# Kernel tuning notes

Measured on AMD Instinct MI355X. Metric: run time of the kernel, lower is better.

## Reference

```python
import jax, jax.numpy as jnp
import numpy as np

B, L, E, H = 2048, 64, 128, 128  # batch, sourceL(=seq_len), lstm input dim (embedding_dim+2), hidden_dim
STEPS = (L - 1) * 2              # decode loop length from Decoder.forward
C_TANH = 10.0                    # tanh_exploration (pointer uses use_tanh=True)
NEG = -1e9                       # stand-in for -inf mask fill (grad-safe)


def setup_inputs() -> dict:
    key = jax.random.key(0)
    ks = jax.random.split(key, 20)
    s = 1.0 / np.sqrt(H)
    u = lambda k, shp: jax.random.uniform(k, shp, minval=-s, maxval=s, dtype=jnp.float32)
    return {
        'decoder_input': jax.random.normal(ks[0], (B, E), dtype=jnp.float32),
        'embedded_inputs': jax.random.normal(ks[1], (L, B, E), dtype=jnp.float32),
        'context': jax.random.normal(ks[2], (L, B, H), dtype=jnp.float32),
        'h0': jax.random.normal(ks[3], (B, H), dtype=jnp.float32),
        'c0': jax.random.normal(ks[4], (B, H), dtype=jnp.float32),
        # nn.LSTM(E, H) single-step cell params (PyTorch gate order i,f,g,o)
        'W_ih': u(ks[5], (4 * H, E)), 'W_hh': u(ks[6], (4 * H, H)),
        'b_ih': u(ks[7], (4 * H,)), 'b_hh': u(ks[8], (4 * H,)),
        # glimpse Attention (use_tanh=False): Linear(dim,dim), Conv1d(dim,dim,1), v
        'g_Wq': u(ks[9], (H, H)), 'g_bq': u(ks[10], (H,)),
        'g_Wref': u(ks[11], (H, H)), 'g_bref': u(ks[12], (H,)),
        'g_v': u(ks[13], (H,)),
        # pointer Attention (use_tanh=True, C=10)
        'p_Wq': u(ks[14], (H, H)), 'p_bq': u(ks[15], (H,)),
        'p_Wref': u(ks[16], (H, H)), 'p_bref': u(ks[17], (H,)),
        'p_v': u(ks[18], (H,)),
    }


def reference(decoder_input, embedded_inputs, context, h0, c0,
              W_ih, W_hh, b_ih, b_hh,
              g_Wq, g_bq, g_Wref, g_bref, g_v,
              p_Wq, p_bq, p_Wref, p_bref, p_v):
    # ref.permute(1,2,0): [sourceL,B,H] -> [B,H,L]; conv1d(dim,dim,1) == per-position linear.
    refT = jnp.transpose(context, (1, 2, 0))                                  # [B,H,L]
    e_g = jnp.einsum('oh,bhl->bol', g_Wref, refT) + g_bref[None, :, None]     # glimpse projected ref
    e_p = jnp.einsum('oh,bhl->bol', p_Wref, refT) + p_bref[None, :, None]     # pointer projected ref
    barange = jnp.arange(B)

    def step(carry, _):
        h, c, mask, idxs, x = carry
        # LSTM cell step (PyTorch i,f,g,o gate order)
        gates = x @ W_ih.T + h @ W_hh.T + (b_ih + b_hh)                       # [B,4H]
        i_, f_, g_, o_ = jnp.split(gates, 4, axis=1)
        c_new = jax.nn.sigmoid(f_) * c + jax.nn.sigmoid(i_) * jnp.tanh(g_)
        h_new = jax.nn.sigmoid(o_) * jnp.tanh(c_new)
        # apply_mask_to_logits: mark prev idxs, unmask depot (col 0) for non-depot prev
        mask = mask.at[barange, idxs].set(True)
        mask = mask.at[:, 0].set(jnp.where(idxs != 0, False, mask[:, 0]))
        # glimpse: additive attention, masked softmax, bmm with projected ref e
        qg = h_new @ g_Wq.T + g_bq                                            # [B,H]
        ug = jnp.einsum('h,bhl->bl', g_v, jnp.tanh(qg[:, :, None] + e_g))     # [B,L]
        ug = jnp.where(mask, NEG, ug)
        g_l = jnp.einsum('bhl,bl->bh', e_g, jax.nn.softmax(ug, axis=1))       # glimpse vector
        # pointer: additive attention with C*tanh, masked softmax
        qp = g_l @ p_Wq.T + p_bq
        up = jnp.einsum('h,bhl->bl', p_v, jnp.tanh(qp[:, :, None] + e_p))
        up = C_TANH * jnp.tanh(up)
        up = jnp.where(mask, NEG, up)
        probs = jax.nn.softmax(up, axis=1)                                    # [B,L]
        # selection (deterministic argmax stand-in for multinomial) + next decoder input
        new_idxs = jnp.argmax(probs, axis=1)
        x_new = embedded_inputs[new_idxs, barange, :]                         # [B,E]
        return (h_new, c_new, mask, new_idxs, x_new), probs

    mask0 = jnp.zeros((B, L), dtype=bool)
    idxs0 = jnp.zeros((B,), dtype=jnp.int32)
    _, probs_seq = jax.lax.scan(step, (h0, c0, mask0, idxs0, decoder_input), None, length=STEPS)
    prob0 = jnp.zeros((B, L), dtype=probs_seq.dtype).at[:, 0].set(1.0)        # initial depot one-hot
    return jnp.concatenate([prob0[None], probs_seq], axis=0)                  # [STEPS+1,B,L]
```

## Files before the change

kernel.cpp:

```cpp
#include <hip/hip_runtime.h>


#define B_ 2048
#define L_ 64
#define H_ 128
#define STEPS_ 126
#define NEGV -1000000000.0f

__device__ __forceinline__ float fast_rcp(float x) { return __builtin_amdgcn_rcpf(x); }
__device__ __forceinline__ float sigm(float x) { return 1.0f / (1.0f + __expf(-x)); }
__device__ __forceinline__ float dot4(float4 a, float4 b) {
  return a.x * b.x + a.y * b.y + a.z * b.z + a.w * b.w;
}

__global__ __launch_bounds__(256) void xw_gemm(const float* __restrict__ A,
                                               const float* __restrict__ W,
                                               const float* __restrict__ b1,
                                               const float* __restrict__ b2,
                                               float* __restrict__ C) {
  __shared__ float As[64][36];
  __shared__ float Ws[64][36];
  const int t = threadIdx.x;
  const int tx = t & 15, ty = t >> 4;
  const long row0 = (long)blockIdx.x * 64;
  const int col0 = blockIdx.y * 64;
  float acc[4][4] = {};
  for (int k0 = 0; k0 < 128; k0 += 32) {
#pragma unroll
    for (int i = 0; i < 2; ++i) {
      int f4 = t * 2 + i;
      int r = f4 >> 3, c = (f4 & 7) * 4;
      *(float4*)&As[r][c] = *(const float4*)&A[(row0 + r) * 128 + k0 + c];
      *(float4*)&Ws[r][c] = *(const float4*)&W[(long)(col0 + r) * 128 + k0 + c];
    }
    __syncthreads();
#pragma unroll
    for (int kk = 0; kk < 32; kk += 4) {
      float4 a[4], w[4];
#pragma unroll
      for (int i = 0; i < 4; ++i) a[i] = *(float4*)&As[ty * 4 + i][kk];
#pragma unroll
      for (int j = 0; j < 4; ++j) w[j] = *(float4*)&Ws[tx * 4 + j][kk];
#pragma unroll
      for (int i = 0; i < 4; ++i)
#pragma unroll
        for (int j = 0; j < 4; ++j)
          acc[i][j] += dot4(a[i], w[j]);
    }
    __syncthreads();
  }
#pragma unroll
  for (int i = 0; i < 4; ++i) {
    long r = row0 + ty * 4 + i;
#pragma unroll
    for (int j = 0; j < 4; ++j) {
      int cc = col0 + tx * 4 + j;
      C[r * 512 + cc] = acc[i][j] + b1[cc] + b2[cc];
    }
  }
}

__global__ __launch_bounds__(512, 1) void ptrnet_main(
    const float* __restrict__ dec, const float* __restrict__ emb,
    const float* __restrict__ ctx, const float* __restrict__ h0,
    const float* __restrict__ c0, const float* __restrict__ W_ih,
    const float* __restrict__ W_hh, const float* __restrict__ b_ih,
    const float* __restrict__ b_hh, const float* __restrict__ gWq,
    const float* __restrict__ gbq, const float* __restrict__ gWref,
    const float* __restrict__ gbref, const float* __restrict__ gv,
    const float* __restrict__ pWq, const float* __restrict__ pbq,
    const float* __restrict__ pWref, const float* __restrict__ pbref,
    const float* __restrict__ pv, const float* __restrict__ XW,
    const float* __restrict__ XW0, float* __restrict__ out, int use_precomp) {
  const int b = blockIdx.x;
  const int t = threadIdx.x;
  const int l = t & 63;
  const int hb = t >> 6;

  __shared__ float tegS[128][64];
  __shared__ float tepS[128][64];
  __shared__ float egT[64][128];
  __shared__ __align__(16) float hS[128];
  __shared__ float cS[128];
  __shared__ __align__(16) float glS[128];
  __shared__ __align__(16) float xS[128];
  __shared__ float gatesS[512];
  __shared__ __align__(16) float aG[128];
  __shared__ __align__(16) float gvaG[128];
  __shared__ __align__(16) float aP[128];
  __shared__ __align__(16) float pvaP[128];
  __shared__ __align__(16) float gvS[128];
  __shared__ __align__(16) float pvS[128];
  __shared__ float gbqS[128], pbqS[128];
  __shared__ float bS[512];
  __shared__ float wS[64];
  __shared__ float part[8][64];
  __shared__ float red4[4][128];
  __shared__ int maskS[64];
  __shared__ int curS;

  if (t < 128) {
    hS[t] = h0[(long)b * 128 + t];
    cS[t] = c0[(long)b * 128 + t];
    gvS[t] = gv[t];
    pvS[t] = pv[t];
    gbqS[t] = gbq[t];
    pbqS[t] = pbq[t];
  }
  bS[t] = b_ih[t] + b_hh[t];
  if (t < 64) {
    maskS[t] = 0;
    out[(long)b * 64 + t] = (t == 0) ? 1.0f : 0.0f;
  }
  if (t == 0) curS = 0;

  {
    const float4* crow4 = (const float4*)(ctx + ((long)l * B_ + b) * 128);
    for (int k = 0; k < 16; ++k) {
      int h = hb * 16 + k;
      float eg = gbref[h], ep = pbref[h];
      const float4* wg4 = (const float4*)(gWref + (long)h * 128);
      const float4* wp4 = (const float4*)(pWref + (long)h * 128);
#pragma unroll
      for (int c = 0; c < 32; ++c) {
        float4 cv = crow4[c];
        eg += dot4(cv, wg4[c]);
        ep += dot4(cv, wp4[c]);
      }
      egT[l][h] = eg;
      tegS[h][l] = tanhf(eg);
      tepS[h][l] = tanhf(ep);
    }
  }

  float4 whh[32];
  const float4* Whh4 = (const float4*)W_hh;
#pragma unroll
  for (int c = 0; c < 32; ++c) whh[c] = Whh4[(long)t * 32 + c];
  float4 qw[16];
  {
    const float4* Q4 = (t < 256) ? (const float4*)gWq : (const float4*)pWq;
    int j = (t & 255) >> 1, half = t & 1;
#pragma unroll
    for (int c = 0; c < 16; ++c) qw[c] = Q4[(long)j * 32 + half * 16 + c];
  }
  __syncthreads();

  const float4* hS4 = (const float4*)hS;
  const float4* glS4 = (const float4*)glS;
  const float4* xS4 = (const float4*)xS;
  float4* xS4w = (float4*)xS;

  for (int step = 0; step < STEPS_; ++step) {
    const int cur = curS;
    if (t == 0) {
      maskS[cur] = 1;
      if (cur != 0) maskS[0] = 0;
    }

    if (!use_precomp) {
      if (t < 32)
        xS4w[t] = (step == 0) ? ((const float4*)(dec + (long)b * 128))[t]
                              : ((const float4*)(emb + ((long)cur * B_ + b) * 128))[t];
      __syncthreads();
    }

    float xv;
    if (use_precomp) {
      const float* xw = (step == 0) ? (XW0 + (long)b * 512)
                                    : (XW + ((long)cur * B_ + b) * 512);
      xv = xw[t];
    } else {
      xv = bS[t];
      const float4* wih4 = (const float4*)(W_ih + (long)t * 128);
#pragma unroll
      for (int c = 0; c < 32; ++c) xv += dot4(wih4[c], xS4[c]);
    }
    {
      float acc = 0.f;
#pragma unroll
      for (int c = 0; c < 32; ++c) acc += dot4(whh[c], hS4[c]);
      gatesS[t] = acc + xv;
    }
    __syncthreads();

    if (t < 128) {
      float gi = gatesS[t], gf = gatesS[t + 128];
      float gg = gatesS[t + 256], go = gatesS[t + 384];
      float cn = sigm(gf) * cS[t] + sigm(gi) * tanhf(gg);
      cS[t] = cn;
      hS[t] = sigm(go) * tanhf(cn);
    }
    __syncthreads();

    if (t < 256) {
      int j = t >> 1, half = t & 1;
      float p = 0.f;
#pragma unroll
      for (int c = 0; c < 16; ++c) p += dot4(qw[c], hS4[half * 16 + c]);
      p += __shfl_xor(p, 1);
      if (half == 0) {
        float a = tanhf(p + gbqS[j]);
        aG[j] = a;
        gvaG[j] = gvS[j] * a;
      }
    }
    __syncthreads();

    {
      const float4* a4 = (const float4*)aG;
      const float4* g4 = (const float4*)gvS;
      const float4* ga4 = (const float4*)gvaG;
      float4 av[4], gv4[4], gav[4];
#pragma unroll
      for (int i = 0; i < 4; ++i) {
        av[i] = a4[hb * 4 + i];
        gv4[i] = g4[hb * 4 + i];
        gav[i] = ga4[hb * 4 + i];
      }
      const float* af = (const float*)av;
      const float* gf = (const float*)gv4;
      const float* gaf = (const float*)gav;
      float sum = 0.f;
#pragma unroll
      for (int k = 0; k < 16; ++k) {
        float te = tegS[hb * 16 + k][l];
        float den = fmaf(af[k], te, 1.0f);
        float n2 = fmaf(gf[k], te, gaf[k]);
        sum = fmaf(n2, fast_rcp(den), sum);
      }
      part[hb][l] = sum;
    }
    __syncthreads();

    if (t < 64) {
      float u = part[0][l] + part[1][l] + part[2][l] + part[3][l] +
                part[4][l] + part[5][l] + part[6][l] + part[7][l];
      if (maskS[l]) u = NEGV;
      float m = u;
#pragma unroll
      for (int d = 32; d; d >>= 1) m = fmaxf(m, __shfl_xor(m, d));
      float e = __expf(u - m);
      float s = e;
#pragma unroll
      for (int d = 32; d; d >>= 1) s += __shfl_xor(s, d);
      wS[l] = e / s;
    }
    __syncthreads();

    {
      int h = t & 127, lh = t >> 7;
      float sum = 0.f;
#pragma unroll
      for (int q = 0; q < 16; ++q) {
        int l2 = lh * 16 + q;
        sum = fmaf(egT[l2][h], wS[l2], sum);
      }
      red4[lh][h] = sum;
    }
    __syncthreads();
    if (t < 128) glS[t] = red4[0][t] + red4[1][t] + red4[2][t] + red4[3][t];
    __syncthreads();

    if (t >= 256) {
      int j = (t - 256) >> 1, half = t & 1;
      float p = 0.f;
#pragma unroll
      for (int c = 0; c < 16; ++c) p += dot4(qw[c], glS4[half * 16 + c]);
      p += __shfl_xor(p, 1);
      if (half == 0) {
        float a = tanhf(p + pbqS[j]);
        aP[j] = a;
        pvaP[j] = pvS[j] * a;
      }
    }
    __syncthreads();

    {
      const float4* a4 = (const float4*)aP;
      const float4* p4 = (const float4*)pvS;
      const float4* pa4 = (const float4*)pvaP;
      float4 av[4], pv4[4], pav[4];
#pragma unroll
      for (int i = 0; i < 4; ++i) {
        av[i] = a4[hb * 4 + i];
        pv4[i] = p4[hb * 4 + i];
        pav[i] = pa4[hb * 4 + i];
      }
      const float* af = (const float*)av;
      const float* pf = (const float*)pv4;
      const float* paf = (const float*)pav;
      float sum = 0.f;
#pragma unroll
      for (int k = 0; k < 16; ++k) {
        float te = tepS[hb * 16 + k][l];
        float den = fmaf(af[k], te, 1.0f);
        float n2 = fmaf(pf[k], te, paf[k]);
        sum = fmaf(n2, fast_rcp(den), sum);
      }
      part[hb][l] = sum;
    }
    __syncthreads();

    if (t < 64) {
      float u = part[0][l] + part[1][l] + part[2][l] + part[3][l] +
                part[4][l] + part[5][l] + part[6][l] + part[7][l];
      u = 10.0f * tanhf(u);
      if (maskS[l]) u = NEGV;
      float m = u;
#pragma unroll
      for (int d = 32; d; d >>= 1) m = fmaxf(m, __shfl_xor(m, d));
      float e = __expf(u - m);
      float s = e;
#pragma unroll
      for (int d = 32; d; d >>= 1) s += __shfl_xor(s, d);
      float p = e / s;
      out[((long)(step + 1) * B_ + b) * 64 + l] = p;
      float bv = p;
      int bi = l;
#pragma unroll
      for (int d = 32; d; d >>= 1) {
        float ov = __shfl_xor(bv, d);
        int oi = __shfl_xor(bi, d);
        if (ov > bv || (ov == bv && oi < bi)) { bv = ov; bi = oi; }
      }
      if (t == 0) curS = bi;
    }
    __syncthreads();
  }
}

extern "C" void kernel_launch(void* const* d_in, const int* in_sizes, int n_in,
                              void* d_out, int out_size, void* d_ws, size_t ws_size,
                              hipStream_t stream) {
  const float* dec = (const float*)d_in[0];
  const float* emb = (const float*)d_in[1];
  const float* ctx = (const float*)d_in[2];
  const float* h0 = (const float*)d_in[3];
  const float* c0 = (const float*)d_in[4];
  const float* Wih = (const float*)d_in[5];
  const float* Whh = (const float*)d_in[6];
  const float* bih = (const float*)d_in[7];
  const float* bhh = (const float*)d_in[8];
  const float* gWq = (const float*)d_in[9];
  const float* gbq = (const float*)d_in[10];
  const float* gWref = (const float*)d_in[11];
  const float* gbref = (const float*)d_in[12];
  const float* gv = (const float*)d_in[13];
  const float* pWq = (const float*)d_in[14];
  const float* pbq = (const float*)d_in[15];
  const float* pWref = (const float*)d_in[16];
  const float* pbref = (const float*)d_in[17];
  const float* pv = (const float*)d_in[18];
  float* out = (float*)d_out;

  const size_t xw_elems = (size_t)L_ * B_ * 512;
  const size_t need = (xw_elems + (size_t)B_ * 512) * sizeof(float);
  const int use_precomp = (ws_size >= need) ? 1 : 0;
  float* XW = (float*)d_ws;
  float* XW0 = XW + xw_elems;

  if (use_precomp) {
    dim3 g1((L_ * B_) / 64, 512 / 64);
    xw_gemm<<<g1, 256, 0, stream>>>(emb, Wih, bih, bhh, XW);
    dim3 g2(B_ / 64, 512 / 64);
    xw_gemm<<<g2, 256, 0, stream>>>(dec, Wih, bih, bhh, XW0);
  }
  ptrnet_main<<<dim3(B_), dim3(512), 0, stream>>>(
      dec, emb, ctx, h0, c0, Wih, Whh, bih, bhh, gWq, gbq, gWref, gbref, gv,
      pWq, pbq, pWref, pbref, pv, XW, XW0, out, use_precomp);
}
```

Baseline: 15.18 ms.

## Double block size to 1024 threads and split per-step dot products across more lanes

Each batch block now runs 1024 threads instead of 512. The LSTM gate products, query projections, attention sums and glimpse reduction are split over twice as many threads, with extra shuffles and shared-memory partial reductions. This cuts per-thread register arrays (whh from 32 to 16 float4) and should shorten the serial critical path of each decode step. The egT row is also padded to 129 to avoid bank conflicts. The cost is more threads per block, which limits concurrent blocks per CU, plus more reduction overhead at each synchronised step.

```diff
diff --git a/kernel.cpp b/kernel.cpp
--- a/kernel.cpp
+++ b/kernel.cpp
@@ -60,7 +60,7 @@
   }
 }
 
-__global__ __launch_bounds__(512, 1) void ptrnet_main(
+__global__ __launch_bounds__(1024) void ptrnet_main(
     const float* __restrict__ dec, const float* __restrict__ emb,
     const float* __restrict__ ctx, const float* __restrict__ h0,
     const float* __restrict__ c0, const float* __restrict__ W_ih,
@@ -74,12 +74,12 @@
     const float* __restrict__ XW0, float* __restrict__ out, int use_precomp) {
   const int b = blockIdx.x;
   const int t = threadIdx.x;
-  const int l = t & 63;
-  const int hb = t >> 6;
+  const int lane = t & 63;
+  const int wid = t >> 6;
 
   __shared__ float tegS[128][64];
   __shared__ float tepS[128][64];
-  __shared__ float egT[64][128];
+  __shared__ float egT[64][129];
   __shared__ __align__(16) float hS[128];
   __shared__ float cS[128];
   __shared__ __align__(16) float glS[128];
@@ -93,9 +93,9 @@
   __shared__ __align__(16) float pvS[128];
   __shared__ float gbqS[128], pbqS[128];
   __shared__ float bS[512];
-  __shared__ float wS[64];
-  __shared__ float part[8][64];
-  __shared__ float red4[4][128];
+  __shared__ __align__(16) float wS[64];
+  __shared__ float part2[16][64];
+  __shared__ float red8[8][128];
   __shared__ int maskS[64];
   __shared__ int curS;
 
@@ -107,7 +107,7 @@
     gbqS[t] = gbq[t];
     pbqS[t] = pbq[t];
   }
-  bS[t] = b_ih[t] + b_hh[t];
+  if (t < 512) bS[t] = b_ih[t] + b_hh[t];
   if (t < 64) {
     maskS[t] = 0;
     out[(long)b * 64 + t] = (t == 0) ? 1.0f : 0.0f;
@@ -115,9 +115,10 @@
   if (t == 0) curS = 0;
 
   {
-    const float4* crow4 = (const float4*)(ctx + ((long)l * B_ + b) * 128);
-    for (int k = 0; k < 16; ++k) {
-      int h = hb * 16 + k;
+    const float4* crow4 = (const float4*)(ctx + ((long)lane * B_ + b) * 128);
+#pragma unroll
+    for (int k = 0; k < 8; ++k) {
+      int h = wid * 8 + k;
       float eg = gbref[h], ep = pbref[h];
       const float4* wg4 = (const float4*)(gWref + (long)h * 128);
       const float4* wp4 = (const float4*)(pWref + (long)h * 128);
@@ -127,22 +128,27 @@
         eg += dot4(cv, wg4[c]);
         ep += dot4(cv, wp4[c]);
       }
-      egT[l][h] = eg;
-      tegS[h][l] = tanhf(eg);
-      tepS[h][l] = tanhf(ep);
-    }
-  }
-
-  float4 whh[32];
-  const float4* Whh4 = (const float4*)W_hh;
-#pragma unroll
-  for (int c = 0; c < 32; ++c) whh[c] = Whh4[(long)t * 32 + c];
-  float4 qw[16];
+      egT[lane][h] = eg;
+      tegS[h][lane] = tanhf(eg);
+      tepS[h][lane] = tanhf(ep);
+    }
+  }
+
+  const int r = t >> 1;
+  const int kh = t & 1;
+  float4 whh[16];
   {
-    const float4* Q4 = (t < 256) ? (const float4*)gWq : (const float4*)pWq;
-    int j = (t & 255) >> 1, half = t & 1;
-#pragma unroll
-    for (int c = 0; c < 16; ++c) qw[c] = Q4[(long)j * 32 + half * 16 + c];
+    const float4* Whh4 = (const float4*)W_hh;
+#pragma unroll
+    for (int c = 0; c < 16; ++c) whh[c] = Whh4[(long)r * 32 + kh * 16 + c];
+  }
+  const int qj = (t & 511) >> 2;
+  const int qk = t & 3;
+  float4 qw[8];
+  {
+    const float4* Q4 = (t < 512) ? (const float4*)gWq : (const float4*)pWq;
+#pragma unroll
+    for (int c = 0; c < 8; ++c) qw[c] = Q4[(long)qj * 32 + qk * 8 + c];
   }
   __syncthreads();
 
@@ -165,22 +171,27 @@
       __syncthreads();
     }
 
-    float xv;
-    if (use_precomp) {
-      const float* xw = (step == 0) ? (XW0 + (long)b * 512)
-                                    : (XW + ((long)cur * B_ + b) * 512);
-      xv = xw[t];
-    } else {
-      xv = bS[t];
-      const float4* wih4 = (const float4*)(W_ih + (long)t * 128);
-#pragma unroll
-      for (int c = 0; c < 32; ++c) xv += dot4(wih4[c], xS4[c]);
-    }
     {
       float acc = 0.f;
 #pragma unroll
-      for (int c = 0; c < 32; ++c) acc += dot4(whh[c], hS4[c]);
-      gatesS[t] = acc + xv;
+      for (int c = 0; c < 16; ++c) acc += dot4(whh[c], hS4[kh * 16 + c]);
+      if (!use_precomp) {
+        const float4* wih4 = (const float4*)(W_ih + (long)r * 128);
+#pragma unroll
+        for (int c = 0; c < 16; ++c) acc += dot4(wih4[kh * 16 + c], xS4[kh * 16 + c]);
+      }
+      acc += __shfl_xor(acc, 1);
+      if (kh == 0) {
+        float xv;
+        if (use_precomp) {
+          const float* xw = (step == 0) ? (XW0 + (long)b * 512)
+                                        : (XW + ((long)cur * B_ + b) * 512);
+          xv = xw[r];
+        } else {
+          xv = bS[r];
+        }
+        gatesS[r] = acc + xv;
+      }
     }
     __syncthreads();
 
@@ -193,16 +204,16 @@
     }
     __syncthreads();
 
-    if (t < 256) {
-      int j = t >> 1, half = t & 1;
+    if (t < 512) {
       float p = 0.f;
 #pragma unroll
-      for (int c = 0; c < 16; ++c) p += dot4(qw[c], hS4[half * 16 + c]);
+      for (int c = 0; c < 8; ++c) p += dot4(qw[c], hS4[qk * 8 + c]);
       p += __shfl_xor(p, 1);
-      if (half == 0) {
-        float a = tanhf(p + gbqS[j]);
-        aG[j] = a;
-        gvaG[j] = gvS[j] * a;
+      p += __shfl_xor(p, 2);
+      if (qk == 0) {
+        float a = tanhf(p + gbqS[qj]);
+        aG[qj] = a;
+        gvaG[qj] = gvS[qj] * a;
       }
     }
     __syncthreads();
@@ -211,32 +222,32 @@
       const float4* a4 = (const float4*)aG;
       const float4* g4 = (const float4*)gvS;
       const float4* ga4 = (const float4*)gvaG;
-      float4 av[4], gv4[4], gav[4];
-#pragma unroll
-      for (int i = 0; i < 4; ++i) {
-        av[i] = a4[hb * 4 + i];
-        gv4[i] = g4[hb * 4 + i];
-        gav[i] = ga4[hb * 4 + i];
-      }
-      const float* af = (const float*)av;
-      const float* gf = (const float*)gv4;
-      const float* gaf = (const float*)gav;
       float sum = 0.f;
 #pragma unroll
-      for (int k = 0; k < 16; ++k) {
-        float te = tegS[hb * 16 + k][l];
-        float den = fmaf(af[k], te, 1.0f);
-        float n2 = fmaf(gf[k], te, gaf[k]);
-        sum = fmaf(n2, fast_rcp(den), sum);
-      }
-      part[hb][l] = sum;
+      for (int ch = 0; ch < 2; ++ch) {
+        float4 av = a4[wid * 2 + ch];
+        float4 gg4 = g4[wid * 2 + ch];
+        float4 gav = ga4[wid * 2 + ch];
+        const float* af = (const float*)&av;
+        const float* gf = (const float*)&gg4;
+        const float* gaf = (const float*)&gav;
+#pragma unroll
+        for (int k = 0; k < 4; ++k) {
+          float te = tegS[wid * 8 + ch * 4 + k][lane];
+          float den = fmaf(af[k], te, 1.0f);
+          float n2 = fmaf(gf[k], te, gaf[k]);
+          sum = fmaf(n2, fast_rcp(den), sum);
+        }
+      }
+      part2[wid][lane] = sum;
     }
     __syncthreads();
 
     if (t < 64) {
-      float u = part[0][l] + part[1][l] + part[2][l] + part[3][l] +
-                part[4][l] + part[5][l] + part[6][l] + part[7][l];
-      if (maskS[l]) u = NEGV;
+      float u = 0.f;
+#pragma unroll
+      for (int i = 0; i < 16; ++i) u += part2[i][t];
+      if (maskS[t]) u = NEGV;
       float m = u;
 #pragma unroll
       for (int d = 32; d; d >>= 1) m = fmaxf(m, __shfl_xor(m, d));
@@ -244,34 +255,42 @@
       float s = e;
 #pragma unroll
       for (int d = 32; d; d >>= 1) s += __shfl_xor(s, d);
-      wS[l] = e / s;
+      wS[t] = e / s;
     }
     __syncthreads();
 
     {
       int h = t & 127, lh = t >> 7;
+      float4 w0 = ((const float4*)wS)[lh * 2];
+      float4 w1 = ((const float4*)wS)[lh * 2 + 1];
+      const float* wf0 = (const float*)&w0;
+      const float* wf1 = (const float*)&w1;
       float sum = 0.f;
 #pragma unroll
-      for (int q = 0; q < 16; ++q) {
-        int l2 = lh * 16 + q;
-        sum = fmaf(egT[l2][h], wS[l2], sum);
-      }
-      red4[lh][h] = sum;
-    }
-    __syncthreads();
-    if (t < 128) glS[t] = red4[0][t] + red4[1][t] + red4[2][t] + red4[3][t];
-    __syncthreads();
-
-    if (t >= 256) {
-      int j = (t - 256) >> 1, half = t & 1;
+      for (int q = 0; q < 4; ++q) sum = fmaf(egT[lh * 8 + q][h], wf0[q], sum);
+#pragma unroll
+      for (int q = 0; q < 4; ++q) sum = fmaf(egT[lh * 8 + 4 + q][h], wf1[q], sum);
+      red8[lh][h] = sum;
+    }
+    __syncthreads();
+    if (t < 128) {
+      float s = 0.f;
+#pragma unroll
+      for (int i = 0; i < 8; ++i) s += red8[i][t];
+      glS[t] = s;
+    }
+    __syncthreads();
+
+    if (t >= 512) {
       float p = 0.f;
 #pragma unroll
-      for (int c = 0; c < 16; ++c) p += dot4(qw[c], glS4[half * 16 + c]);
+      for (int c = 0; c < 8; ++c) p += dot4(qw[c], glS4[qk * 8 + c]);
       p += __shfl_xor(p, 1);
-      if (half == 0) {
-        float a = tanhf(p + pbqS[j]);
-        aP[j] = a;
-        pvaP[j] = pvS[j] * a;
+      p += __shfl_xor(p, 2);
+      if (qk == 0) {
+        float a = tanhf(p + pbqS[qj]);
+        aP[qj] = a;
+        pvaP[qj] = pvS[qj] * a;
       }
     }
     __syncthreads();
@@ -280,33 +299,33 @@
       const float4* a4 = (const float4*)aP;
       const float4* p4 = (const float4*)pvS;
       const float4* pa4 = (const float4*)pvaP;
-      float4 av[4], pv4[4], pav[4];
-#pragma unroll
-      for (int i = 0; i < 4; ++i) {
-        av[i] = a4[hb * 4 + i];
-        pv4[i] = p4[hb * 4 + i];
-        pav[i] = pa4[hb * 4 + i];
-      }
-      const float* af = (const float*)av;
-      const float* pf = (const float*)pv4;
-      const float* paf = (const float*)pav;
       float sum = 0.f;
 #pragma unroll
-      for (int k = 0; k < 16; ++k) {
-        float te = tepS[hb * 16 + k][l];
-        float den = fmaf(af[k], te, 1.0f);
-        float n2 = fmaf(pf[k], te, paf[k]);
-        sum = fmaf(n2, fast_rcp(den), sum);
-      }
-      part[hb][l] = sum;
+      for (int ch = 0; ch < 2; ++ch) {
+        float4 av = a4[wid * 2 + ch];
+        float4 pp4 = p4[wid * 2 + ch];
+        float4 pav = pa4[wid * 2 + ch];
+        const float* af = (const float*)&av;
+        const float* pf = (const float*)&pp4;
+        const float* paf = (const float*)&pav;
+#pragma unroll
+        for (int k = 0; k < 4; ++k) {
+          float te = tepS[wid * 8 + ch * 4 + k][lane];
+          float den = fmaf(af[k], te, 1.0f);
+          float n2 = fmaf(pf[k], te, paf[k]);
+          sum = fmaf(n2, fast_rcp(den), sum);
+        }
+      }
+      part2[wid][lane] = sum;
     }
     __syncthreads();
 
     if (t < 64) {
-      float u = part[0][l] + part[1][l] + part[2][l] + part[3][l] +
-                part[4][l] + part[5][l] + part[6][l] + part[7][l];
+      float u = 0.f;
+#pragma unroll
+      for (int i = 0; i < 16; ++i) u += part2[i][t];
       u = 10.0f * tanhf(u);
-      if (maskS[l]) u = NEGV;
+      if (maskS[t]) u = NEGV;
       float m = u;
 #pragma unroll
       for (int d = 32; d; d >>= 1) m = fmaxf(m, __shfl_xor(m, d));
@@ -315,9 +334,9 @@
 #pragma unroll
       for (int d = 32; d; d >>= 1) s += __shfl_xor(s, d);
       float p = e / s;
-      out[((long)(step + 1) * B_ + b) * 64 + l] = p;
+      out[((long)(step + 1) * B_ + b) * 64 + t] = p;
       float bv = p;
-      int bi = l;
+      int bi = t;
 #pragma unroll
       for (int d = 32; d; d >>= 1) {
         float ov = __shfl_xor(bv, d);
@@ -366,7 +385,7 @@
     dim3 g2(B_ / 64, 512 / 64);
     xw_gemm<<<g2, 256, 0, stream>>>(dec, Wih, bih, bhh, XW0);
   }
-  ptrnet_main<<<dim3(B_), dim3(512), 0, stream>>>(
+  ptrnet_main<<<dim3(B_), dim3(1024), 0, stream>>>(
       dec, emb, ctx, h0, c0, Wih, Whh, bih, bhh, gWq, gbq, gWref, gbref, gv,
       pWq, pbq, pWref, pbref, pv, XW, XW0, out, use_precomp);
 }
```

Measured after the change: 26.16 ms. 1.72x slower.

## Stream transposed W_hh from memory to cut registers and allow two blocks per CU

Applied to the files above, without the earlier changes.

The 128 float4 registers per thread that held W_hh are removed. W_hh is now transposed once into workspace and streamed coalesced from global/L2 each step, with hS read as broadcasts from shared memory. The query projections are split across all 512 threads, four lanes per output combined with shuffles, and the launch-bounds min-blocks hint is dropped so occupancy can rise. egT is padded to 129 columns to avoid shared-memory bank conflicts. The trade-off is repeated global reads of W_hh at every step in exchange for lower register pressure.

```diff
diff --git a/kernel.cpp b/kernel.cpp
--- a/kernel.cpp
+++ b/kernel.cpp
@@ -60,7 +60,14 @@
   }
 }
 
-__global__ __launch_bounds__(512, 1) void ptrnet_main(
+__global__ __launch_bounds__(256) void whh_transpose(const float* __restrict__ W,
+                                                     float* __restrict__ WT) {
+  int idx = blockIdx.x * 256 + threadIdx.x;
+  int j = idx >> 7, k = idx & 127;
+  WT[k * 512 + j] = W[j * 128 + k];
+}
+
+__global__ __launch_bounds__(512) void ptrnet_main(
     const float* __restrict__ dec, const float* __restrict__ emb,
     const float* __restrict__ ctx, const float* __restrict__ h0,
     const float* __restrict__ c0, const float* __restrict__ W_ih,
@@ -71,7 +78,8 @@
     const float* __restrict__ pWq, const float* __restrict__ pbq,
     const float* __restrict__ pWref, const float* __restrict__ pbref,
     const float* __restrict__ pv, const float* __restrict__ XW,
-    const float* __restrict__ XW0, float* __restrict__ out, int use_precomp) {
+    const float* __restrict__ XW0, const float* __restrict__ WT,
+    float* __restrict__ out, int use_precomp) {
   const int b = blockIdx.x;
   const int t = threadIdx.x;
   const int l = t & 63;
@@ -79,7 +87,7 @@
 
   __shared__ float tegS[128][64];
   __shared__ float tepS[128][64];
-  __shared__ float egT[64][128];
+  __shared__ float egT[64][129];
   __shared__ __align__(16) float hS[128];
   __shared__ float cS[128];
   __shared__ __align__(16) float glS[128];
@@ -133,16 +141,17 @@
     }
   }
 
-  float4 whh[32];
-  const float4* Whh4 = (const float4*)W_hh;
-#pragma unroll
-  for (int c = 0; c < 32; ++c) whh[c] = Whh4[(long)t * 32 + c];
-  float4 qw[16];
+  const int qj = t >> 2;
+  const int qk = t & 3;
+  float4 qwg[8], qwp[8];
   {
-    const float4* Q4 = (t < 256) ? (const float4*)gWq : (const float4*)pWq;
-    int j = (t & 255) >> 1, half = t & 1;
-#pragma unroll
-    for (int c = 0; c < 16; ++c) qw[c] = Q4[(long)j * 32 + half * 16 + c];
+    const float4* G4 = (const float4*)gWq;
+    const float4* P4 = (const float4*)pWq;
+#pragma unroll
+    for (int c = 0; c < 8; ++c) {
+      qwg[c] = G4[(long)qj * 32 + qk * 8 + c];
+      qwp[c] = P4[(long)qj * 32 + qk * 8 + c];
+    }
   }
   __syncthreads();
 
@@ -158,29 +167,33 @@
       if (cur != 0) maskS[0] = 0;
     }
 
-    if (!use_precomp) {
+    if (use_precomp) {
+      const float* xw = (step == 0) ? (XW0 + (long)b * 512)
+                                    : (XW + ((long)cur * B_ + b) * 512);
+      float xv = xw[t];
+      float a0 = 0.f, a1 = 0.f, a2 = 0.f, a3 = 0.f;
+#pragma unroll 8
+      for (int k = 0; k < 128; k += 4) {
+        a0 = fmaf(WT[(k + 0) * 512 + t], hS[k + 0], a0);
+        a1 = fmaf(WT[(k + 1) * 512 + t], hS[k + 1], a1);
+        a2 = fmaf(WT[(k + 2) * 512 + t], hS[k + 2], a2);
+        a3 = fmaf(WT[(k + 3) * 512 + t], hS[k + 3], a3);
+      }
+      gatesS[t] = (a0 + a1) + (a2 + a3) + xv;
+    } else {
       if (t < 32)
         xS4w[t] = (step == 0) ? ((const float4*)(dec + (long)b * 128))[t]
                               : ((const float4*)(emb + ((long)cur * B_ + b) * 128))[t];
       __syncthreads();
-    }
-
-    float xv;
-    if (use_precomp) {
-      const float* xw = (step == 0) ? (XW0 + (long)b * 512)
-                                    : (XW + ((long)cur * B_ + b) * 512);
-      xv = xw[t];
-    } else {
-      xv = bS[t];
+      float acc = bS[t];
       const float4* wih4 = (const float4*)(W_ih + (long)t * 128);
-#pragma unroll
-      for (int c = 0; c < 32; ++c) xv += dot4(wih4[c], xS4[c]);
-    }
-    {
-      float acc = 0.f;
-#pragma unroll
-      for (int c = 0; c < 32; ++c) acc += dot4(whh[c], hS4[c]);
-      gatesS[t] = acc + xv;
+      const float4* whh4 = (const float4*)(W_hh + (long)t * 128);
+#pragma unroll
+      for (int c = 0; c < 32; ++c) {
+        acc += dot4(wih4[c], xS4[c]);
+        acc += dot4(whh4[c], hS4[c]);
+      }
+      gatesS[t] = acc;
     }
     __syncthreads();
 
@@ -193,16 +206,16 @@
     }
     __syncthreads();
 
-    if (t < 256) {
-      int j = t >> 1, half = t & 1;
+    {
       float p = 0.f;
 #pragma unroll
-      for (int c = 0; c < 16; ++c) p += dot4(qw[c], hS4[half * 16 + c]);
+      for (int c = 0; c < 8; ++c) p += dot4(qwg[c], hS4[qk * 8 + c]);
       p += __shfl_xor(p, 1);
-      if (half == 0) {
-        float a = tanhf(p + gbqS[j]);
-        aG[j] = a;
-        gvaG[j] = gvS[j] * a;
+      p += __shfl_xor(p, 2);
+      if (qk == 0) {
+        float a = tanhf(p + gbqS[qj]);
+        aG[qj] = a;
+        gvaG[qj] = gvS[qj] * a;
       }
     }
     __syncthreads();
@@ -262,16 +275,16 @@
     if (t < 128) glS[t] = red4[0][t] + red4[1][t] + red4[2][t] + red4[3][t];
     __syncthreads();
 
-    if (t >= 256) {
-      int j = (t - 256) >> 1, half = t & 1;
+    {
       float p = 0.f;
 #pragma unroll
-      for (int c = 0; c < 16; ++c) p += dot4(qw[c], glS4[half * 16 + c]);
+      for (int c = 0; c < 8; ++c) p += dot4(qwp[c], glS4[qk * 8 + c]);
       p += __shfl_xor(p, 1);
-      if (half == 0) {
-        float a = tanhf(p + pbqS[j]);
-        aP[j] = a;
-        pvaP[j] = pvS[j] * a;
+      p += __shfl_xor(p, 2);
+      if (qk == 0) {
+        float a = tanhf(p + pbqS[qj]);
+        aP[qj] = a;
+        pvaP[qj] = pvS[qj] * a;
       }
     }
     __syncthreads();
@@ -355,18 +368,22 @@
   float* out = (float*)d_out;
 
   const size_t xw_elems = (size_t)L_ * B_ * 512;
-  const size_t need = (xw_elems + (size_t)B_ * 512) * sizeof(float);
+  const size_t x0_elems = (size_t)B_ * 512;
+  const size_t wt_elems = (size_t)512 * 128;
+  const size_t need = (xw_elems + x0_elems + wt_elems) * sizeof(float);
   const int use_precomp = (ws_size >= need) ? 1 : 0;
   float* XW = (float*)d_ws;
   float* XW0 = XW + xw_elems;
+  float* WT = XW0 + x0_elems;
 
   if (use_precomp) {
     dim3 g1((L_ * B_) / 64, 512 / 64);
     xw_gemm<<<g1, 256, 0, stream>>>(emb, Wih, bih, bhh, XW);
     dim3 g2(B_ / 64, 512 / 64);
     xw_gemm<<<g2, 256, 0, stream>>>(dec, Wih, bih, bhh, XW0);
+    whh_transpose<<<256, 256, 0, stream>>>(Whh, WT);
   }
   ptrnet_main<<<dim3(B_), dim3(512), 0, stream>>>(
       dec, emb, ctx, h0, c0, Wih, Whh, bih, bhh, gWq, gbq, gWref, gbref, gv,
-      pWq, pbq, pWref, pbref, pv, XW, XW0, out, use_precomp);
-}
+      pWq, pbq, pWref, pbref, pv, XW, XW0, WT, out, use_precomp);
+}
```

New measurement: 19.67 ms. 29.6% more time.
